# Performance work log

Hardware: AMD Instinct MI355X
Metric: run time of the kernel (lower is better)

## Reference

```python
import jax, jax.numpy as jnp
import numpy as np

# Module hyperparameters (see init_kwargs)
P1, P2 = 32, 32      # num_patches_h, num_patches_w (256/8)
H1, W2 = 8, 8        # patch_size
CH = 3               # input channels
CI, SI = 768, 4      # num_cores, rfs_per_capsule (capsule_size=256, rf_size=64)
KOUT, LOUT = 256, 4  # output_cores, slots per output core
PROBA = 0.1          # connection_proba


def setup_inputs() -> dict:
    key = jax.random.key(0)
    kx, kc = jax.random.split(key)
    x = jax.random.normal(kx, (128, 256, 256, 3), dtype=jnp.float32)
    # fast_scrramble: fixed random-sparse binary connectivity tensor
    # [source_core, source_slot, dest_core, dest_slot]
    C = jax.random.bernoulli(kc, PROBA, (CI, SI, KOUT, LOUT)).astype(jnp.float32)
    return {"x": x, "C": C}


def reference(x, C):
    b = x.shape[0]
    # 'b (p1 h1) (p2 w2) c -> b p1 p2 h1 w2 c'
    x = x.reshape(b, P1, H1, P2, W2, CH).transpose(0, 1, 3, 2, 4, 5)
    # 'b p1 p2 h1 w2 c -> b h1 w2 (p1 p2 c)'
    x = x.transpose(0, 3, 4, 1, 2, 5).reshape(b, H1, W2, P1 * P2 * CH)
    # 'b h1 w2 (ci si) -> b ci si h1 w2'
    x = x.reshape(b, H1, W2, CI, SI).transpose(0, 3, 4, 1, 2)
    # Literal einsum from the source: no shared labels between operands,
    # so this is sum_{c,s} x (per b,h,w) times sum_{i,j} C (per k,l).
    return jnp.einsum('bcshw,ijkl->bklhw', x, C)
```

## Files before the change

kernel.cpp:

```cpp
#include <hip/hip_runtime.h>


typedef float nf4 __attribute__((ext_vector_type(4)));

__global__ __launch_bounds__(192, 3) void reduce_partials(
    const float4* __restrict__ x4,
    const float4* __restrict__ C4,
    float*  __restrict__ cpart,
    float*  __restrict__ sxf)
{
    const int t   = threadIdx.x;
    const int blk = blockIdx.x;

    if (blk >= 1024) {
        const int cb = blk - 1024;
        const size_t r0 = (size_t)cb * 32;
        for (int c4 = t; c4 < 256; c4 += 192) {
            const float4* p = C4 + r0 * 256 + c4;
            float ax = 0, ay = 0, az = 0, aw = 0;
            float bx = 0, by = 0, bz = 0, bw = 0;
#pragma unroll
            for (int r = 0; r < 32; r += 2) {
                float4 v0 = p[0];
                float4 v1 = p[256];
                ax += v0.x; ay += v0.y; az += v0.z; aw += v0.w;
                bx += v1.x; by += v1.y; bz += v1.z; bw += v1.w;
                p += 512;
            }
            float4 s;
            s.x = ax + bx; s.y = ay + by; s.z = az + bz; s.w = aw + bw;
            ((float4*)cpart)[cb * 256 + c4] = s;
        }
        return;
    }

    const int b = blk >> 3;
    const int h = blk & 7;
    const nf4* base = (const nf4*)(x4 + ((size_t)b * 256 + h) * 192 + t);

    nf4 acc = (nf4)(0.f);
#pragma unroll
    for (int j = 0; j < 32; ++j) {
        nf4 v = __builtin_nontemporal_load(&base[(size_t)j * 8 * 192]);
        acc += v;
    }

    __shared__ float4 arr[192];
    __shared__ float4 arr2[48];
    __shared__ float  cls[24];

    arr[t].x = acc.x; arr[t].y = acc.y; arr[t].z = acc.z; arr[t].w = acc.w;
    __syncthreads();

    if (t < 48) {
        float4 a0 = arr[t], a1 = arr[t + 48], a2 = arr[t + 96], a3 = arr[t + 144];
        float4 s;
        s.x = a0.x + a1.x + a2.x + a3.x;
        s.y = a0.y + a1.y + a2.y + a3.y;
        s.z = a0.z + a1.z + a2.z + a3.z;
        s.w = a0.w + a1.w + a2.w + a3.w;
        arr2[t] = s;
    }
    __syncthreads();

    if (t < 6) {
        float4 s; s.x = s.y = s.z = s.w = 0.f;
#pragma unroll
        for (int g = 0; g < 8; ++g) {
            float4 v = arr2[t + 6 * g];
            s.x += v.x; s.y += v.y; s.z += v.z; s.w += v.w;
        }
        cls[4 * t + 0] = s.x;
        cls[4 * t + 1] = s.y;
        cls[4 * t + 2] = s.z;
        cls[4 * t + 3] = s.w;
    }
    __syncthreads();

    if (t < 8) {
        sxf[b * 64 + h * 8 + t] = cls[3 * t] + cls[3 * t + 1] + cls[3 * t + 2];
    }
}

__global__ __launch_bounds__(192) void collapse_C(
    const float* __restrict__ cpart,
    float* __restrict__ scf)
{
    const int col = blockIdx.x * 192 + threadIdx.x;
    if (col < 1024) {
        float s = 0.f;
#pragma unroll 8
        for (int g = 0; g < 96; ++g) s += cpart[g * 1024 + col];
        scf[col] = s;
    }
}

__global__ __launch_bounds__(256) void expand_out(
    const float* __restrict__ sxf,
    const float* __restrict__ scf,
    float4* __restrict__ out4)
{
    const int t   = threadIdx.x;
    const int klc = blockIdx.x;
    const int b   = blockIdx.y;

    __shared__ float4 sxv[16];
    __shared__ float  scl[128];

    if (t < 16) {
        sxv[t] = ((const float4*)(sxf + b * 64))[t];
    } else if (t >= 64 && t < 192) {
        scl[t - 64] = scf[klc * 128 + (t - 64)];
    }
    __syncthreads();

    float4* ob = out4 + (size_t)b * 16384 + (size_t)klc * 2048;
#pragma unroll
    for (int k = 0; k < 8; ++k) {
        const int idx = k * 256 + t;
        const float4 v = sxv[idx & 15];
        const float  s = scl[idx >> 4];
        nf4 r;
        r.x = v.x * s; r.y = v.y * s; r.z = v.z * s; r.w = v.w * s;
        __builtin_nontemporal_store(r, (nf4*)&ob[idx]);
    }
}

extern "C" void kernel_launch(void* const* d_in, const int* in_sizes, int n_in,
                              void* d_out, int out_size, void* d_ws, size_t ws_size,
                              hipStream_t stream) {
    const float4* x4 = (const float4*)d_in[0];
    const float4* C4 = (const float4*)d_in[1];

    float* cpart = (float*)d_ws;
    float* sxf   = cpart + 96 * 1024;
    float* scf   = sxf + 128 * 64;

    reduce_partials<<<dim3(1024 + 96), 192, 0, stream>>>(x4, C4, cpart, sxf);
    collapse_C<<<dim3(6),              192, 0, stream>>>(cpart, scf);
    expand_out<<<dim3(8, 128),         256, 0, stream>>>(sxf, scf, (float4*)d_out);
}
```

Before: 167.1 us.

## Split x reduction into half-image blocks and schedule C blocks first

New measurement: 174.0 us. +4.1%, slower.

```diff
diff --git a/kernel.cpp b/kernel.cpp
--- a/kernel.cpp
+++ b/kernel.cpp
@@ -3,18 +3,17 @@
 
 typedef float nf4 __attribute__((ext_vector_type(4)));
 
-__global__ __launch_bounds__(192, 3) void reduce_partials(
+__global__ __launch_bounds__(192, 6) void reduce_partials(
     const float4* __restrict__ x4,
     const float4* __restrict__ C4,
     float*  __restrict__ cpart,
-    float*  __restrict__ sxf)
+    float*  __restrict__ xh)
 {
     const int t   = threadIdx.x;
     const int blk = blockIdx.x;
 
-    if (blk >= 1024) {
-        const int cb = blk - 1024;
-        const size_t r0 = (size_t)cb * 32;
+    if (blk < 96) {
+        const size_t r0 = (size_t)blk * 32;
         for (int c4 = t; c4 < 256; c4 += 192) {
             const float4* p = C4 + r0 * 256 + c4;
             float ax = 0, ay = 0, az = 0, aw = 0;
@@ -29,20 +28,23 @@
             }
             float4 s;
             s.x = ax + bx; s.y = ay + by; s.z = az + bz; s.w = aw + bw;
-            ((float4*)cpart)[cb * 256 + c4] = s;
+            ((float4*)cpart)[blk * 256 + c4] = s;
         }
         return;
     }
 
-    const int b = blk >> 3;
-    const int h = blk & 7;
-    const nf4* base = (const nf4*)(x4 + ((size_t)b * 256 + h) * 192 + t);
+    const int task = blk - 96;
+    const int b    = task >> 4;
+    const int rem  = task & 15;
+    const int h    = rem >> 1;
+    const int half = rem & 1;
+    const float4* base = x4 + ((size_t)b * 256 + h + 128 * half) * 192 + t;
 
     nf4 acc = (nf4)(0.f);
 #pragma unroll
-    for (int j = 0; j < 32; ++j) {
-        nf4 v = __builtin_nontemporal_load(&base[(size_t)j * 8 * 192]);
-        acc += v;
+    for (int j = 0; j < 16; ++j) {
+        const float4 v = base[(size_t)j * 8 * 192];
+        acc.x += v.x; acc.y += v.y; acc.z += v.z; acc.w += v.w;
     }
 
     __shared__ float4 arr[192];
@@ -78,7 +80,7 @@
     __syncthreads();
 
     if (t < 8) {
-        sxf[b * 64 + h * 8 + t] = cls[3 * t] + cls[3 * t + 1] + cls[3 * t + 2];
+        xh[task * 8 + t] = cls[3 * t] + cls[3 * t + 1] + cls[3 * t + 2];
     }
 }
 
@@ -96,7 +98,7 @@
 }
 
 __global__ __launch_bounds__(256) void expand_out(
-    const float* __restrict__ sxf,
+    const float* __restrict__ xh,
     const float* __restrict__ scf,
     float4* __restrict__ out4)
 {
@@ -104,12 +106,13 @@
     const int klc = blockIdx.x;
     const int b   = blockIdx.y;
 
-    __shared__ float4 sxv[16];
-    __shared__ float  scl[128];
+    __shared__ float sxs[64];
+    __shared__ float scl[128];
 
-    if (t < 16) {
-        sxv[t] = ((const float4*)(sxf + b * 64))[t];
-    } else if (t >= 64 && t < 192) {
+    if (t < 64) {
+        const float* p = xh + b * 128 + (t >> 3) * 16 + (t & 7);
+        sxs[t] = p[0] + p[8];
+    } else if (t < 192) {
         scl[t - 64] = scf[klc * 128 + (t - 64)];
     }
     __syncthreads();
@@ -118,7 +121,7 @@
 #pragma unroll
     for (int k = 0; k < 8; ++k) {
         const int idx = k * 256 + t;
-        const float4 v = sxv[idx & 15];
+        const float4 v = ((const float4*)sxs)[idx & 15];
         const float  s = scl[idx >> 4];
         nf4 r;
         r.x = v.x * s; r.y = v.y * s; r.z = v.z * s; r.w = v.w * s;
@@ -133,10 +136,10 @@
     const float4* C4 = (const float4*)d_in[1];
 
     float* cpart = (float*)d_ws;
-    float* sxf   = cpart + 96 * 1024;
-    float* scf   = sxf + 128 * 64;
+    float* xh    = cpart + 96 * 1024;
+    float* scf   = xh + 16384;
 
-    reduce_partials<<<dim3(1024 + 96), 192, 0, stream>>>(x4, C4, cpart, sxf);
+    reduce_partials<<<dim3(96 + 2048), 192, 0, stream>>>(x4, C4, cpart, xh);
     collapse_C<<<dim3(6),              192, 0, stream>>>(cpart, scf);
-    expand_out<<<dim3(8, 128),         256, 0, stream>>>(sxf, scf, (float4*)d_out);
+    expand_out<<<dim3(8, 128),         256, 0, stream>>>(xh, scf, (float4*)d_out);
 }
```
